# Performance work log

Measured on AMD Instinct MI355X. Metric: run time of the kernel, lower is better.

## Reference

```python
import jax, jax.numpy as jnp
import numpy as np

B, M, L, D, H, DFF, K, NL = 32, 512, 512, 128, 8, 256, 16, 2


def setup_inputs() -> dict:
    key = jax.random.key(0)
    ks = jax.random.split(key, 12)
    s = 0.02
    p = lambda i, shape: (jax.random.normal(ks[i], shape, jnp.float32) * s)
    return {
        "enc_out_vari": jax.random.normal(ks[0], (B, M, D), jnp.float32),
        "x_enc": jax.random.normal(ks[1], (B, L, M), jnp.float32),
        "conv1_W": p(2, (D, D)), "conv1_b": jnp.zeros((D,), jnp.float32),
        "conv2_W": p(3, (D, D)), "conv2_b": jnp.zeros((D,), jnp.float32),
        "Wq": p(4, (NL, D, D)), "Wk": p(5, (NL, D, D)),
        "Wv": p(6, (NL, D, D)), "Wo": p(7, (NL, D, D)),
        "ffn_W1": p(8, (NL, D, DFF)), "ffn_b1": jnp.zeros((NL, DFF), jnp.float32),
        "ffn_W2": p(9, (NL, DFF, D)), "ffn_b2": jnp.zeros((NL, D), jnp.float32),
        "ln1_g": jnp.ones((NL, D), jnp.float32), "ln1_b": jnp.zeros((NL, D), jnp.float32),
        "ln2_g": jnp.ones((NL, D), jnp.float32), "ln2_b": jnp.zeros((NL, D), jnp.float32),
    }


def _ln(x, g, b, eps=1e-5):
    mu = x.mean(-1, keepdims=True)
    var = ((x - mu) ** 2).mean(-1, keepdims=True)
    return (x - mu) * jax.lax.rsqrt(var + eps) * g + b


def _gcn_conv(x, src, dst, W, b, N):
    # PyG GCNConv: XW, add self loops, symmetric D^-1/2 (A+I) D^-1/2 aggregation, + bias
    h = x @ W
    loop = jnp.arange(N)
    s = jnp.concatenate([src, loop])
    d = jnp.concatenate([dst, loop])
    deg = jax.ops.segment_sum(jnp.ones_like(d, jnp.float32), d, num_segments=N)
    dinv = jnp.where(deg > 0, jax.lax.rsqrt(deg), 0.0)
    norm = dinv[s] * dinv[d]
    out = jax.ops.segment_sum(h[s] * norm[:, None], d, num_segments=N)
    return out + b


def _forward(enc_out_vari, x_enc, conv1_W, conv1_b, conv2_W, conv2_b,
             Wq, Wk, Wv, Wo, ffn_W1, ffn_b1, ffn_W2, ffn_b2,
             ln1_g, ln1_b, ln2_g, ln2_b):
    # --- dynamic graph from Pearson correlation (faithful: ascending argsort, idx 1..k) ---
    x = x_enc.transpose(0, 2, 1)                      # [B, M, L]
    c = x - x.mean(-1, keepdims=True)
    cov = jnp.einsum('bml,bnl->bmn', c, c) / (L - 1)  # [B, M, M]
    std = jnp.sqrt(jnp.diagonal(cov, axis1=-2, axis2=-1))
    std = jnp.where(std == 0, 1.0, std)
    corr = cov / (std[:, :, None] * std[:, None, :])
    neighbors = jnp.argsort(corr, axis=-1)[:, :, 1:K + 1]  # [B, M, K]
    row = jnp.tile(jnp.arange(M), K)                  # arange(M).repeat(k) in torch
    col = neighbors.reshape(B, M * K)
    offs = (jnp.arange(B) * M)[:, None]               # batch the graphs into one
    src = (row[None, :] + offs).reshape(-1)
    dst = (col + offs).reshape(-1)
    N = B * M
    # --- 2-layer GCN over flattened node set ---
    x_raw = enc_out_vari.reshape(N, D)
    h1 = jax.nn.relu(_gcn_conv(x_raw, src, dst, conv1_W, conv1_b, N))
    h2 = jax.nn.relu(_gcn_conv(h1, src, dst, conv2_W, conv2_b, N))
    xg = h2.reshape(B, M, D)
    # --- cross-attention transformer encoder: query stream = enc_out_vari, kv = GCN output ---
    h = enc_out_vari
    hd = D // H
    scale = 1.0 / jnp.sqrt(jnp.float32(hd))
    for l in range(NL):
        q = (h @ Wq[l]).reshape(B, M, H, hd)
        k_ = (xg @ Wk[l]).reshape(B, M, H, hd)
        v = (xg @ Wv[l]).reshape(B, M, H, hd)
        att = jax.nn.softmax(jnp.einsum('bqhd,bkhd->bhqk', q, k_) * scale, axis=-1)
        o = jnp.einsum('bhqk,bkhd->bqhd', att, v).reshape(B, M, D) @ Wo[l]
        h = _ln(h + o, ln1_g[l], ln1_b[l])
        f = jax.nn.relu(h @ ffn_W1[l] + ffn_b1[l]) @ ffn_W2[l] + ffn_b2[l]
        h = _ln(h + f, ln2_g[l], ln2_b[l])
    return h


def reference(enc_out_vari, x_enc, conv1_W, conv1_b, conv2_W, conv2_b,
              Wq, Wk, Wv, Wo, ffn_W1, ffn_b1, ffn_W2, ffn_b2,
              ln1_g, ln1_b, ln2_g, ln2_b):
    return _forward(enc_out_vari, x_enc, conv1_W, conv1_b, conv2_W, conv2_b,
                    Wq, Wk, Wv, Wo, ffn_W1, ffn_b1, ffn_W2, ffn_b2,
                    ln1_g, ln1_b, ln2_g, ln2_b)
```

## Files before the change

### kernel.cpp

```cpp
#include <hip/hip_runtime.h>
#include <float.h>

#define BB 32
#define MMv 512
#define LLv 512
#define DDv 128
#define HHv 8
#define DFFv 256
#define KNB 16
#define NLAY 2
#define NNODE (BB*MMv)
#define TOTE  (NNODE*KNB)
#define WTOT  294912

typedef unsigned short ushort_t;
typedef unsigned int u32;
typedef __attribute__((ext_vector_type(8))) short bf16x8;
typedef __attribute__((ext_vector_type(4))) float f32x4;

__device__ __forceinline__ float bf2f(ushort_t u){
  union { u32 i; float f; } x; x.i = ((u32)u) << 16; return x.f;
}
__device__ __forceinline__ ushort_t f2bf(float f){
  union { u32 i; float f; } x; x.f = f;
  u32 r = x.i + 0x7FFFu + ((x.i >> 16) & 1u);
  return (ushort_t)(r >> 16);
}
__device__ __forceinline__ float ldx(const void* p, size_t i, int f32){
  return f32 ? ((const float*)p)[i] : bf2f(((const ushort_t*)p)[i]);
}
__device__ __forceinline__ float wsum(float v){
  #pragma unroll
  for(int s=32;s;s>>=1) v += __shfl_xor(v,s);
  return v;
}

__global__ __launch_bounds__(256) void diag_fill_k(float* out, int n, float val){
  for(int i = blockIdx.x*256 + threadIdx.x; i < n; i += gridDim.x*256) out[i] = val;
}

struct P18 { const ushort_t* p[18]; int n[18]; };
__global__ __launch_bounds__(256) void ddet_k(P18 a, int* DF){
  int i = blockIdx.x;
  const ushort_t* q = a.p[i];
  int P = min(a.n[i], 4096);
  int t = threadIdx.x;
  int r1 = 0, evenNZ = 0, oddNZ = 0;
  for(int j=t; j<P; j+=256){
    ushort_t v = q[j];
    if(((v >> 7) & 0xFF) >= 0xC0) r1 = 1;
    if(v){ if(j & 1) oddNZ = 1; else evenNZ = 1; }
  }
  __shared__ int sh[3];
  if(t==0){ sh[0]=0; sh[1]=0; sh[2]=0; }
  __syncthreads();
  if(r1) atomicOr(&sh[0],1);
  if(evenNZ) atomicOr(&sh[1],1);
  if(oddNZ) atomicOr(&sh[2],1);
  __syncthreads();
  if(t==0) DF[i] = sh[0] | ((sh[1]==0) & (sh[2]!=0));
}

__global__ __launch_bounds__(256) void prep_k(const void* c1W, const void* c2W,
    const void* Wq, const void* Wk, const void* Wv, const void* Wo,
    const void* W1, const void* W2, ushort_t* Wth, ushort_t* Wtl, const int* DF){
  __shared__ ushort_t th[32][33];
  __shared__ ushort_t tl[32][33];
  int job = blockIdx.z;
  const void* src; int dfi; size_t soff, doff; int K, N;
  switch(job){
    case 0:  src=c1W; dfi=2;  soff=0; K=128; N=128; doff=0; break;
    case 1:  src=c2W; dfi=4;  soff=0; K=128; N=128; doff=16384; break;
    case 2: case 3:
      src=Wq; dfi=6; soff=(size_t)(job-2)*16384; K=128; N=128;
      doff=32768 + (size_t)(job-2)*16384; break;
    case 4: case 5:
      src=Wk; dfi=7; soff=(size_t)(job-4)*16384; K=128; N=128;
      doff=65536 + (size_t)(job-4)*16384; break;
    case 6: case 7:
      src=Wv; dfi=8; soff=(size_t)(job-6)*16384; K=128; N=128;
      doff=98304 + (size_t)(job-6)*16384; break;
    case 8: case 9:
      src=Wo; dfi=9; soff=(size_t)(job-8)*16384; K=128; N=128;
      doff=131072 + (size_t)(job-8)*16384; break;
    case 10: case 11:
      src=W1; dfi=10; soff=(size_t)(job-10)*32768; K=128; N=256;
      doff=163840 + (size_t)(job-10)*32768; break;
    default:
      src=W2; dfi=12; soff=(size_t)(job-12)*32768; K=256; N=128;
      doff=229376 + (size_t)(job-12)*32768; break;
  }
  int n0 = blockIdx.x*32, k0 = blockIdx.y*32;
  if(n0 >= N || k0 >= K) return;
  int f32 = DF[dfi];
  int tx = threadIdx.x, ty = threadIdx.y;
  #pragma unroll
  for(int i=0;i<4;i++){
    int k = k0+ty+8*i, n = n0+tx;
    float x = ldx(src, soff + (size_t)k*N + n, f32);
    ushort_t hi = f2bf(x);
    ushort_t lo = f2bf(x - bf2f(hi));
    th[ty+8*i][tx] = hi; tl[ty+8*i][tx] = lo;
  }
  __syncthreads();
  #pragma unroll
  for(int i=0;i<4;i++){
    int n = n0+ty+8*i, k = k0+tx;
    size_t d = doff + (size_t)n*K + k;
    Wth[d] = th[tx][ty+8*i];
    Wtl[d] = tl[tx][ty+8*i];
  }
}

__global__ __launch_bounds__(256) void split_k(const void* xe, ushort_t* Xhi,
                                               ushort_t* Xlo, const int* DF){
  __shared__ ushort_t th[32][33];
  __shared__ ushort_t tl[32][33];
  int f32 = DF[1];
  int b = blockIdx.z;
  int m0 = blockIdx.x*32, l0 = blockIdx.y*32;
  int tx = threadIdx.x, ty = threadIdx.y;
  #pragma unroll
  for(int i=0;i<4;i++){
    int l = l0+ty+8*i, m = m0+tx;
    float x = ldx(xe, (size_t)b*LLv*MMv + (size_t)l*MMv + m, f32);
    ushort_t hi = f2bf(x);
    ushort_t lo = f2bf(x - bf2f(hi));
    th[ty+8*i][tx] = hi; tl[ty+8*i][tx] = lo;
  }
  __syncthreads();
  #pragma unroll
  for(int i=0;i<4;i++){
    size_t d = (size_t)b*MMv*LLv + (size_t)(m0+ty+8*i)*LLv + l0+tx;
    Xhi[d] = th[tx][ty+8*i];
    Xlo[d] = tl[tx][ty+8*i];
  }
}

__global__ __launch_bounds__(256) void stats2_k(const ushort_t* Xhi, const ushort_t* Xlo,
                                                double* S64, double* R64){
  int row = blockIdx.x*4 + (threadIdx.x >> 6);
  int lane = threadIdx.x & 63;
  const ushort_t* Hr = Xhi + (size_t)row*LLv + lane*8;
  const ushort_t* Lr = Xlo + (size_t)row*LLv + lane*8;
  float s = 0.f, ss = 0.f;
  #pragma unroll
  for(int j=0;j<8;j++){
    float x = bf2f(Hr[j]) + bf2f(Lr[j]);
    s += x; ss = fmaf(x, x, ss);
  }
  s = wsum(s); ss = wsum(ss);
  if(lane == 0){
    S64[row] = (double)s;
    float cov = (ss - s*s*(1.0f/LLv)) * (1.0f/(LLv-1));
    float sd = (cov > 0.f) ? sqrtf(cov) : 0.f;
    R64[row] = (sd > 0.f) ? (double)(1.0f/sd) : 1.0;
  }
}

__global__ __launch_bounds__(1024) void corrsel_k(const ushort_t* Xhi, const ushort_t* Xlo,
                                                  const double* S64, const double* R64,
                                                  int* nbr, const int* DF){
  __shared__ __attribute__((aligned(16))) ushort_t Ah[32*520];
  __shared__ __attribute__((aligned(16))) ushort_t Al[32*520];
  __shared__ float Cs[32*516];
  int f32 = DF[1];
  int lin = blockIdx.y*16 + blockIdx.x;
  int xcd = lin & 7, slot = lin >> 3;
  int b = xcd + 8*(slot >> 4);
  int strip = slot & 15;
  int m0 = strip*32;
  int t = threadIdx.x;
  int wave = t >> 6, lane = t & 63;
  int quad = lane >> 4, l16 = lane & 15;
  const ushort_t* Hb = Xhi + (size_t)b*MMv*LLv;
  const ushort_t* Lb = Xlo + (size_t)b*MMv*LLv;
  for(int idx=t; idx<2048; idx+=1024){
    int mm = idx >> 6, c8 = (idx & 63)*8;
    *(bf16x8*)&Ah[mm*520 + c8] = *(const bf16x8*)&Hb[(size_t)(m0+mm)*LLv + c8];
    *(bf16x8*)&Al[mm*520 + c8] = *(const bf16x8*)&Lb[(size_t)(m0+mm)*LLv + c8];
  }
  __syncthreads();
  const double* Sb = S64 + b*MMv;
  const double* Rb = R64 + b*MMv;
  int nbase = wave*32;
  for(int cs=0; cs<2; cs++){
    int nn = nbase + cs*16 + l16;
    size_t brow = (size_t)nn*LLv + quad*8;
    f32x4 a00={0.f,0.f,0.f,0.f}, a01={0.f,0.f,0.f,0.f}, a02={0.f,0.f,0.f,0.f};
    f32x4 a10={0.f,0.f,0.f,0.f}, a11={0.f,0.f,0.f,0.f}, a12={0.f,0.f,0.f,0.f};
    if(f32){
      #pragma unroll
      for(int g=0; g<4; g++){
        bf16x8 bh[4], bl[4];
        #pragma unroll
        for(int j=0;j<4;j++) bh[j] = *(const bf16x8*)&Hb[brow + g*128 + j*32];
        #pragma unroll
        for(int j=0;j<4;j++) bl[j] = *(const bf16x8*)&Lb[brow + g*128 + j*32];
        #pragma unroll
        for(int j=0;j<4;j++){
          int ko = g*128 + j*32 + quad*8;
          bf16x8 ah0 = *(const bf16x8*)&Ah[l16*520 + ko];
          bf16x8 al0 = *(const bf16x8*)&Al[l16*520 + ko];
          bf16x8 ah1 = *(const bf16x8*)&Ah[(16+l16)*520 + ko];
          bf16x8 al1 = *(const bf16x8*)&Al[(16+l16)*520 + ko];
          a00 = __builtin_amdgcn_mfma_f32_16x16x32_bf16(ah0, bh[j], a00, 0, 0, 0);
          a01 = __builtin_amdgcn_mfma_f32_16x16x32_bf16(ah0, bl[j], a01, 0, 0, 0);
          a02 = __builtin_amdgcn_mfma_f32_16x16x32_bf16(al0, bh[j], a02, 0, 0, 0);
          a10 = __builtin_amdgcn_mfma_f32_16x16x32_bf16(ah1, bh[j], a10, 0, 0, 0);
          a11 = __builtin_amdgcn_mfma_f32_16x16x32_bf16(ah1, bl[j], a11, 0, 0, 0);
          a12 = __builtin_amdgcn_mfma_f32_16x16x32_bf16(al1, bh[j], a12, 0, 0, 0);
        }
      }
    } else {
      #pragma unroll
      for(int g=0; g<2; g++){
        bf16x8 bh[8];
        #pragma unroll
        for(int j=0;j<8;j++) bh[j] = *(const bf16x8*)&Hb[brow + g*256 + j*32];
        #pragma unroll
        for(int j=0;j<8;j++){
          int ko = g*256 + j*32 + quad*8;
          bf16x8 ah0 = *(const bf16x8*)&Ah[l16*520 + ko];
          bf16x8 ah1 = *(const bf16x8*)&Ah[(16+l16)*520 + ko];
          if(j & 1){
            a01 = __builtin_amdgcn_mfma_f32_16x16x32_bf16(ah0, bh[j], a01, 0, 0, 0);
            a11 = __builtin_amdgcn_mfma_f32_16x16x32_bf16(ah1, bh[j], a11, 0, 0, 0);
          } else {
            a00 = __builtin_amdgcn_mfma_f32_16x16x32_bf16(ah0, bh[j], a00, 0, 0, 0);
            a10 = __builtin_amdgcn_mfma_f32_16x16x32_bf16(ah1, bh[j], a10, 0, 0, 0);
          }
        }
      }
    }
    float sn = (float)(Sb[nn]*(1.0/LLv));
    float rn = (float)Rb[nn];
    #pragma unroll
    for(int r=0;r<4;r++){
      int ml0 = quad*4 + r;
      float s0 = a00[r] + a01[r] + a02[r];
      float cov0 = (s0 - (float)Sb[m0+ml0]*sn) * (1.0f/(LLv-1));
      Cs[ml0*516 + nn] = cov0 * (float)Rb[m0+ml0] * rn;
      int ml1 = 16 + ml0;
      float s1 = a10[r] + a11[r] + a12[r];
      float cov1 = (s1 - (float)Sb[m0+ml1]*sn) * (1.0f/(LLv-1));
      Cs[ml1*516 + nn] = cov1 * (float)Rb[m0+ml1] * rn;
    }
  }
  __syncthreads();
  for(int rr=0; rr<2; rr++){
    int r = wave*2 + rr;
    float vals[8];
    #pragma unroll
    for(int j=0;j<8;j++) vals[j] = Cs[r*516 + lane + 64*j];
    for(int it=0; it<=KNB; it++){
      float bvv = FLT_MAX; int bi = 0x7fffffff;
      #pragma unroll
      for(int j=0;j<8;j++){
        int n = lane + 64*j;
        if(vals[j] < bvv){ bvv = vals[j]; bi = n; }
      }
      #pragma unroll
      for(int s=32; s; s>>=1){
        float v2 = __shfl_xor(bvv, s);
        int   i2 = __shfl_xor(bi,  s);
        if(v2 < bvv || (v2 == bvv && i2 < bi)){ bvv = v2; bi = i2; }
      }
      int gbi = bi;
      int bic = min(max(gbi, 0), MMv-1);
      if(it > 0 && lane == 0) nbr[(size_t)(b*MMv + m0 + r)*KNB + it-1] = bic;
      if((gbi & 63) == lane && gbi < MMv){
        int jj = gbi >> 6;
        #pragma unroll
        for(int j=0;j<8;j++) if(j == jj) vals[j] = FLT_MAX;
      }
    }
  }
}

__global__ __launch_bounds__(256) void zero_k(int* p){
  p[blockIdx.x*256 + threadIdx.x] = 0;
}

__global__ __launch_bounds__(256) void hist_k(const int* nbr, int* cnt){
  int tid = blockIdx.x*256 + threadIdx.x;
  int b = tid >> 13;
  int col = min(max(nbr[tid], 0), MMv-1);
  atomicAdd(&cnt[b*MMv + col], 1);
}

__global__ __launch_bounds__(256) void scan_k(const int* cnt, int* off,
                                              int* cursor, float* dinv){
  __shared__ int part[256];
  int t = threadIdx.x;
  int base = t*64, s = 0;
  for(int i=0;i<64;i++) s += cnt[base+i];
  part[t] = s; __syncthreads();
  for(int st=1; st<256; st<<=1){
    int v = (t >= st) ? part[t-st] : 0;
    __syncthreads();
    part[t] += v; __syncthreads();
  }
  int run = (t > 0) ? part[t-1] : 0;
  for(int i=0;i<64;i++){
    int idx = base+i;
    off[idx] = run; cursor[idx] = run;
    run += cnt[idx];
    dinv[idx] = 1.0f/sqrtf((float)(cnt[idx]+1));
  }
  if(t == 255) off[NNODE] = run;
}

__global__ __launch_bounds__(256) void fill_k(const int* nbr, int* cursor, int* esrc){
  int tid = blockIdx.x*256 + threadIdx.x;
  int b = tid >> 13;
  int rem = tid & 8191;
  int col = min(max(nbr[tid], 0), MMv-1);
  int dst = b*MMv + col;
  int srcl = rem & 511;
  int pos = atomicAdd(&cursor[dst], 1);
  pos = min(max(pos, 0), TOTE-1);
  esrc[pos] = b*MMv + srcl;
}

__global__ __launch_bounds__(256) void gemm_k(const float* A,
                                              const ushort_t* Wth, const ushort_t* Wtl,
                                              size_t woffT, int wdi,
                                              const void* bias, int boff, int bdi,
                                              float* C, int Kd, int Dout, int relu,
                                              const int* DF){
  __shared__ __attribute__((aligned(16))) ushort_t Ah[64*72];
  __shared__ __attribute__((aligned(16))) ushort_t Al[64*72];
  __shared__ __attribute__((aligned(16))) ushort_t Wh[64*72];
  __shared__ __attribute__((aligned(16))) ushort_t Wl[64*72];
  int wf32 = DF[wdi];
  int bf32 = DF[bdi];
  int m0 = blockIdx.y*64, n0 = blockIdx.x*64;
  int t = threadIdx.x;
  int wave = t >> 6, lane = t & 63;
  int quad = lane >> 4, l16 = lane & 15;
  f32x4 acc[4];
  #pragma unroll
  for(int nt=0;nt<4;nt++) acc[nt] = (f32x4){0.f,0.f,0.f,0.f};
  for(int kc=0; kc<Kd; kc+=64){
    for(int s=t; s<1024; s+=256){
      int row = s >> 4, c4 = (s & 15)*4;
      float4 av = *(const float4*)&A[(size_t)(m0+row)*Kd + kc + c4];
      ushort_t h0=f2bf(av.x), h1=f2bf(av.y), h2=f2bf(av.z), h3=f2bf(av.w);
      ushort_t g0=f2bf(av.x-bf2f(h0)), g1=f2bf(av.y-bf2f(h1));
      ushort_t g2=f2bf(av.z-bf2f(h2)), g3=f2bf(av.w-bf2f(h3));
      *(ushort4*)&Ah[row*72 + c4] = make_ushort4(h0,h1,h2,h3);
      *(ushort4*)&Al[row*72 + c4] = make_ushort4(g0,g1,g2,g3);
    }
    for(int s=t; s<512; s+=256){
      int row = s >> 3, c8 = (s & 7)*8;
      size_t g = woffT + (size_t)(n0+row)*Kd + kc + c8;
      *(bf16x8*)&Wh[row*72 + c8] = *(const bf16x8*)&Wth[g];
      if(wf32) *(bf16x8*)&Wl[row*72 + c8] = *(const bf16x8*)&Wtl[g];
    }
    __syncthreads();
    #pragma unroll
    for(int kk=0; kk<64; kk+=32){
      int ko = kk + quad*8;
      bf16x8 ah = *(const bf16x8*)&Ah[(wave*16+l16)*72 + ko];
      bf16x8 al = *(const bf16x8*)&Al[(wave*16+l16)*72 + ko];
      #pragma unroll
      for(int nt=0; nt<4; nt++){
        bf16x8 wh = *(const bf16x8*)&Wh[(nt*16+l16)*72 + ko];
        acc[nt] = __builtin_amdgcn_mfma_f32_16x16x32_bf16(ah, wh, acc[nt], 0, 0, 0);
        acc[nt] = __builtin_amdgcn_mfma_f32_16x16x32_bf16(al, wh, acc[nt], 0, 0, 0);
        if(wf32){
          bf16x8 wl = *(const bf16x8*)&Wl[(nt*16+l16)*72 + ko];
          acc[nt] = __builtin_amdgcn_mfma_f32_16x16x32_bf16(ah, wl, acc[nt], 0, 0, 0);
        }
      }
    }
    __syncthreads();
  }
  #pragma unroll
  for(int nt=0; nt<4; nt++){
    int n = n0 + nt*16 + l16;
    float bv = bias ? ldx(bias, boff + n, bf32) : 0.f;
    #pragma unroll
    for(int r=0; r<4; r++){
      float v = acc[nt][r] + bv;
      if(relu) v = fmaxf(v, 0.f);
      C[(size_t)(m0 + wave*16 + quad*4 + r)*Dout + n] = v;
    }
  }
}

__global__ __launch_bounds__(256) void agg_k(const float* xw, const int* off,
                                             const int* esrc, const float* dinv,
                                             const void* bias, int bdi, float* out,
                                             const int* DF){
  int f32 = DF[bdi];
  int node = blockIdx.x*4 + (threadIdx.x >> 6);
  int lane = threadIdx.x & 63;
  float dn = dinv[node];
  float2 xv = ((const float2*)(xw + (size_t)node*DDv))[lane];
  float a0 = dn*dn*xv.x;
  float a1 = dn*dn*xv.y;
  int e0 = min(max(off[node], 0), TOTE);
  int e1 = min(max(off[node+1], e0), TOTE);
  for(int e=e0; e<e1; e++){
    int s = min(max(esrc[e], 0), NNODE-1);
    float w = dinv[s]*dn;
    float2 sv = ((const float2*)(xw + (size_t)s*DDv))[lane];
    a0 = fmaf(w, sv.x, a0);
    a1 = fmaf(w, sv.y, a1);
  }
  a0 += ldx(bias, 2*lane, f32); a1 += ldx(bias, 2*lane+1, f32);
  ((float2*)(out + (size_t)node*DDv))[lane] = make_float2(fmaxf(a0,0.f), fmaxf(a1,0.f));
}

__global__ __launch_bounds__(512) void attn_k(const float* qg, const float* kg,
                                              const float* vg, float* og){
  __shared__ float Ks[512*16];
  __shared__ float Vs[512*16];
  int bh = blockIdx.x;
  int b = bh >> 3, hh = bh & 7;
  size_t base = (size_t)b*MMv*DDv + (size_t)hh*16;
  int t = threadIdx.x;
  for(int idx=t; idx<2048; idx+=512){
    int kk = idx >> 2, i4 = (idx & 3)*4;
    ((float4*)Ks)[idx] = *(const float4*)&kg[base + (size_t)kk*DDv + i4];
    ((float4*)Vs)[idx] = *(const float4*)&vg[base + (size_t)kk*DDv + i4];
  }
  __syncthreads();
  int r = t;
  float qr[16];
  #pragma unroll
  for(int i4=0;i4<4;i4++){
    float4 qv = *(const float4*)&qg[base + (size_t)r*DDv + i4*4];
    qr[i4*4+0]=qv.x; qr[i4*4+1]=qv.y; qr[i4*4+2]=qv.z; qr[i4*4+3]=qv.w;
  }
  float m = -FLT_MAX, l = 0.f;
  float acc[16] = {};
  for(int kk=0; kk<512; kk++){
    const float* kp = &Ks[kk*16];
    float s = 0.f;
    #pragma unroll
    for(int i=0;i<16;i++) s = fmaf(qr[i], kp[i], s);
    s *= 0.25f;
    if(s > m){
      float c = __expf(m - s);
      l *= c;
      #pragma unroll
      for(int i=0;i<16;i++) acc[i] *= c;
      m = s;
    }
    float p = __expf(s - m);
    l += p;
    const float* vp = &Vs[kk*16];
    #pragma unroll
    for(int i=0;i<16;i++) acc[i] = fmaf(p, vp[i], acc[i]);
  }
  float inv = 1.0f/l;
  #pragma unroll
  for(int i=0;i<16;i++) og[base + (size_t)r*DDv + i] = acc[i]*inv;
}

__global__ __launch_bounds__(256) void ln_k(const float* h, const float* delta,
                                            const void* g, int gdi, const void* bb, int bdi, int po,
                                            float* dst, const int* DF){
  int gf32 = DF[gdi], bf32 = DF[bdi];
  int row = blockIdx.x*4 + (threadIdx.x >> 6);
  int lane = threadIdx.x & 63;
  const float2* hr = (const float2*)(h + (size_t)row*DDv);
  const float2* dr = (const float2*)(delta + (size_t)row*DDv);
  float2 hv = hr[lane], dv = dr[lane];
  float x0 = hv.x + dv.x, x1 = hv.y + dv.y;
  float mu = wsum(x0 + x1) * (1.0f/DDv);
  float d0 = x0 - mu, d1 = x1 - mu;
  float var = wsum(d0*d0 + d1*d1) * (1.0f/DDv);
  float rs = 1.0f/sqrtf(var + 1e-5f);
  int c0 = lane*2;
  float y0 = d0*rs*ldx(g, po+c0,   gf32) + ldx(bb, po+c0,   bf32);
  float y1 = d1*rs*ldx(g, po+c0+1, gf32) + ldx(bb, po+c0+1, bf32);
  ((float2*)(dst + (size_t)row*DDv))[lane] = make_float2(y0, y1);
}

__global__ __launch_bounds__(256) void cvt_k(const void* in, float* out, const int* DF){
  int f32 = DF[0];
  int tid = blockIdx.x*256 + threadIdx.x;
  out[tid] = ldx(in, tid, f32);
}

extern "C" void kernel_launch(void* const* d_in, const int* in_sizes, int n_in,
                              void* d_out, int out_size, void* d_ws, size_t ws_size,
                              hipStream_t stream) {
  if(n_in != 18){
    diag_fill_k<<<256, 256, 0, stream>>>((float*)d_out, out_size, 1000.0f);
    return;
  }
  const int expect[18] = {
    BB*MMv*DDv, BB*LLv*MMv, DDv*DDv, DDv, DDv*DDv, DDv,
    NLAY*DDv*DDv, NLAY*DDv*DDv, NLAY*DDv*DDv, NLAY*DDv*DDv,
    NLAY*DDv*DFFv, NLAY*DFFv, NLAY*DFFv*DDv, NLAY*DDv,
    NLAY*DDv, NLAY*DDv, NLAY*DDv, NLAY*DDv
  };
  for(int i=0;i<18;i++){
    if(in_sizes[i] != expect[i]){
      diag_fill_k<<<256, 256, 0, stream>>>((float*)d_out, out_size, 2000.0f + 10.0f*i);
      return;
    }
  }

  const void* enc  = d_in[0];
  const void* xe   = d_in[1];
  const void* c1W  = d_in[2];
  const void* c1b  = d_in[3];
  const void* c2W  = d_in[4];
  const void* c2b  = d_in[5];
  const void* Wq   = d_in[6];
  const void* Wk   = d_in[7];
  const void* Wv   = d_in[8];
  const void* Wo   = d_in[9];
  const void* W1   = d_in[10];
  const void* b1   = d_in[11];
  const void* W2   = d_in[12];
  const void* b2   = d_in[13];
  const void* ln1g = d_in[14];
  const void* ln1b = d_in[15];
  const void* ln2g = d_in[16];
  const void* ln2b = d_in[17];

  char* ws = (char*)d_ws;
  size_t o = 0;
  auto alloc = [&](size_t bytes){ size_t r = o; o = (o + bytes + 255) & ~(size_t)255; return r; };
  double* S64  = (double*)(ws + alloc((size_t)NNODE*8));
  double* R64  = (double*)(ws + alloc((size_t)NNODE*8));
  float* dinv  = (float*)(ws + alloc((size_t)NNODE*4));
  int*   cnt   = (int*)  (ws + alloc((size_t)NNODE*4));
  int*   cursor= (int*)  (ws + alloc((size_t)NNODE*4));
  int*   off   = (int*)  (ws + alloc((size_t)(NNODE+1)*4));
  int*   nbr   = (int*)  (ws + alloc((size_t)TOTE*4));
  int*   esrc  = (int*)  (ws + alloc((size_t)TOTE*4));
  int*   DF    = (int*)  (ws + alloc(256));
  ushort_t* Wth = (ushort_t*)(ws + alloc((size_t)WTOT*2));
  ushort_t* Wtl = (ushort_t*)(ws + alloc((size_t)WTOT*2));
  const size_t ACTF = (size_t)NNODE*DDv*4;
  float* hF = (float*)(ws + alloc(ACTF));
  float* xg = (float*)(ws + alloc(ACTF));
  float* t0 = (float*)(ws + alloc(ACTF));
  float* t1 = (float*)(ws + alloc(ACTF));
  float* t2 = (float*)(ws + alloc(ACTF));
  float* t3 = (float*)(ws + alloc(ACTF));
  float* fb = t1;
  ushort_t* Xhi = (ushort_t*)hF;
  ushort_t* Xlo = Xhi + (size_t)BB*MMv*LLv;
  if(ws_size < o){
    diag_fill_k<<<256, 256, 0, stream>>>((float*)d_out, out_size, 3000.0f);
    return;
  }

  P18 pack;
  for(int i=0;i<18;i++){ pack.p[i] = (const ushort_t*)d_in[i]; pack.n[i] = in_sizes[i]; }
  ddet_k<<<18, 256, 0, stream>>>(pack, DF);
  prep_k<<<dim3(8,8,14), dim3(32,8), 0, stream>>>(c1W, c2W, Wq, Wk, Wv, Wo, W1, W2,
                                                  Wth, Wtl, DF);

  split_k<<<dim3(16,16,BB), dim3(32,8), 0, stream>>>(xe, Xhi, Xlo, DF);
  stats2_k<<<NNODE/4, 256, 0, stream>>>(Xhi, Xlo, S64, R64);
  corrsel_k<<<dim3(16, BB), 1024, 0, stream>>>(Xhi, Xlo, S64, R64, nbr, DF);
  zero_k<<<NNODE/256, 256, 0, stream>>>(cnt);
  hist_k<<<TOTE/256, 256, 0, stream>>>(nbr, cnt);
  scan_k<<<1, 256, 0, stream>>>(cnt, off, cursor, dinv);
  fill_k<<<TOTE/256, 256, 0, stream>>>(nbr, cursor, esrc);

  cvt_k<<<NNODE*DDv/256, 256, 0, stream>>>(enc, hF, DF);
  gemm_k<<<dim3(2,256), 256, 0, stream>>>(hF, Wth, Wtl, 0, 2, nullptr, 0, 3, t0, DDv, DDv, 0, DF);
  agg_k<<<NNODE/4, 256, 0, stream>>>(t0, off, esrc, dinv, c1b, 3, t1, DF);
  gemm_k<<<dim3(2,256), 256, 0, stream>>>(t1, Wth, Wtl, 16384, 4, nullptr, 0, 5, t0, DDv, DDv, 0, DF);
  agg_k<<<NNODE/4, 256, 0, stream>>>(t0, off, esrc, dinv, c2b, 5, xg, DF);

  for(int l=0; l<NLAY; l++){
    gemm_k<<<dim3(2,256), 256, 0, stream>>>(hF, Wth, Wtl, 32768 + (size_t)l*16384, 6, nullptr, 0, 6, t0, DDv, DDv, 0, DF);
    gemm_k<<<dim3(2,256), 256, 0, stream>>>(xg, Wth, Wtl, 65536 + (size_t)l*16384, 7, nullptr, 0, 7, t1, DDv, DDv, 0, DF);
    gemm_k<<<dim3(2,256), 256, 0, stream>>>(xg, Wth, Wtl, 98304 + (size_t)l*16384, 8, nullptr, 0, 8, t2, DDv, DDv, 0, DF);
    attn_k<<<BB*HHv, 512, 0, stream>>>(t0, t1, t2, t3);
    gemm_k<<<dim3(2,256), 256, 0, stream>>>(t3, Wth, Wtl, 131072 + (size_t)l*16384, 9, nullptr, 0, 9, t0, DDv, DDv, 0, DF);
    ln_k<<<NNODE/4, 256, 0, stream>>>(hF, t0, ln1g, 14, ln1b, 15, l*DDv, hF, DF);
    gemm_k<<<dim3(4,256), 256, 0, stream>>>(hF, Wth, Wtl, 163840 + (size_t)l*32768, 10, b1, l*DFFv, 11, fb, DDv, DFFv, 1, DF);
    gemm_k<<<dim3(2,256), 256, 0, stream>>>(fb, Wth, Wtl, 229376 + (size_t)l*32768, 12, b2, l*DDv, 13, t0, DFFv, DDv, 0, DF);
    float* dst = (l == NLAY-1) ? (float*)d_out : hF;
    ln_k<<<NNODE/4, 256, 0, stream>>>(hF, t0, ln2g, 16, ln2b, 17, l*DDv, dst, DF);
  }
}
```

Measured before the change: 799.7 us.

## Fuse Q/K/V projections into one GEMM launch with interleaved KV layout

```diff
diff --git a/kernel.cpp b/kernel.cpp
--- a/kernel.cpp
+++ b/kernel.cpp
@@ -73,13 +73,13 @@
     case 1:  src=c2W; dfi=4;  soff=0; K=128; N=128; doff=16384; break;
     case 2: case 3:
       src=Wq; dfi=6; soff=(size_t)(job-2)*16384; K=128; N=128;
-      doff=32768 + (size_t)(job-2)*16384; break;
+      doff=32768 + (size_t)(job-2)*49152; break;
     case 4: case 5:
       src=Wk; dfi=7; soff=(size_t)(job-4)*16384; K=128; N=128;
-      doff=65536 + (size_t)(job-4)*16384; break;
+      doff=32768 + (size_t)(job-4)*49152 + 16384; break;
     case 6: case 7:
       src=Wv; dfi=8; soff=(size_t)(job-6)*16384; K=128; N=128;
-      doff=98304 + (size_t)(job-6)*16384; break;
+      doff=32768 + (size_t)(job-6)*49152 + 32768; break;
     case 8: case 9:
       src=Wo; dfi=9; soff=(size_t)(job-8)*16384; K=128; N=128;
       doff=131072 + (size_t)(job-8)*16384; break;
@@ -390,6 +390,72 @@
   }
 }
 
+__global__ __launch_bounds__(256) void qkv_k(const float* hF, const float* xg,
+                                             const ushort_t* Wth, const ushort_t* Wtl,
+                                             size_t qoff, float* t0, float* kv,
+                                             const int* DF){
+  __shared__ __attribute__((aligned(16))) ushort_t Ah[64*72];
+  __shared__ __attribute__((aligned(16))) ushort_t Al[64*72];
+  __shared__ __attribute__((aligned(16))) ushort_t Wh[64*72];
+  __shared__ __attribute__((aligned(16))) ushort_t Wl[64*72];
+  int m0 = blockIdx.y*64, n0 = blockIdx.x*64;
+  int wdi = (n0 < 128) ? 6 : ((n0 < 256) ? 7 : 8);
+  int wf32 = DF[wdi];
+  const float* A = (n0 < 128) ? hF : xg;
+  int t = threadIdx.x;
+  int wave = t >> 6, lane = t & 63;
+  int quad = lane >> 4, l16 = lane & 15;
+  f32x4 acc[4];
+  #pragma unroll
+  for(int nt=0;nt<4;nt++) acc[nt] = (f32x4){0.f,0.f,0.f,0.f};
+  for(int kc=0; kc<DDv; kc+=64){
+    for(int s=t; s<1024; s+=256){
+      int row = s >> 4, c4 = (s & 15)*4;
+      float4 av = *(const float4*)&A[(size_t)(m0+row)*DDv + kc + c4];
+      ushort_t h0=f2bf(av.x), h1=f2bf(av.y), h2=f2bf(av.z), h3=f2bf(av.w);
+      ushort_t g0=f2bf(av.x-bf2f(h0)), g1=f2bf(av.y-bf2f(h1));
+      ushort_t g2=f2bf(av.z-bf2f(h2)), g3=f2bf(av.w-bf2f(h3));
+      *(ushort4*)&Ah[row*72 + c4] = make_ushort4(h0,h1,h2,h3);
+      *(ushort4*)&Al[row*72 + c4] = make_ushort4(g0,g1,g2,g3);
+    }
+    for(int s=t; s<512; s+=256){
+      int row = s >> 3, c8 = (s & 7)*8;
+      size_t g = qoff + (size_t)(n0+row)*DDv + kc + c8;
+      *(bf16x8*)&Wh[row*72 + c8] = *(const bf16x8*)&Wth[g];
+      if(wf32) *(bf16x8*)&Wl[row*72 + c8] = *(const bf16x8*)&Wtl[g];
+    }
+    __syncthreads();
+    #pragma unroll
+    for(int kk=0; kk<64; kk+=32){
+      int ko = kk + quad*8;
+      bf16x8 ah = *(const bf16x8*)&Ah[(wave*16+l16)*72 + ko];
+      bf16x8 al = *(const bf16x8*)&Al[(wave*16+l16)*72 + ko];
+      #pragma unroll
+      for(int nt=0; nt<4; nt++){
+        bf16x8 wh = *(const bf16x8*)&Wh[(nt*16+l16)*72 + ko];
+        acc[nt] = __builtin_amdgcn_mfma_f32_16x16x32_bf16(ah, wh, acc[nt], 0, 0, 0);
+        acc[nt] = __builtin_amdgcn_mfma_f32_16x16x32_bf16(al, wh, acc[nt], 0, 0, 0);
+        if(wf32){
+          bf16x8 wl = *(const bf16x8*)&Wl[(nt*16+l16)*72 + ko];
+          acc[nt] = __builtin_amdgcn_mfma_f32_16x16x32_bf16(ah, wl, acc[nt], 0, 0, 0);
+        }
+      }
+    }
+    __syncthreads();
+  }
+  float* C = (n0 < 128) ? t0 : kv;
+  int ldC = (n0 < 128) ? 128 : 256;
+  int nb  = (n0 < 128) ? n0 : (n0 - 128);
+  #pragma unroll
+  for(int nt=0; nt<4; nt++){
+    int n = nb + nt*16 + l16;
+    #pragma unroll
+    for(int r=0; r<4; r++){
+      C[(size_t)(m0 + wave*16 + quad*4 + r)*ldC + n] = acc[nt][r];
+    }
+  }
+}
+
 __global__ __launch_bounds__(256) void agg_k(const float* xw, const int* off,
                                              const int* esrc, const float* dinv,
                                              const void* bias, int bdi, float* out,
@@ -403,7 +469,23 @@
   float a1 = dn*dn*xv.y;
   int e0 = min(max(off[node], 0), TOTE);
   int e1 = min(max(off[node+1], e0), TOTE);
-  for(int e=e0; e<e1; e++){
+  int e = e0;
+  for(; e + 4 <= e1; e += 4){
+    int s0 = min(max(esrc[e+0], 0), NNODE-1);
+    int s1 = min(max(esrc[e+1], 0), NNODE-1);
+    int s2 = min(max(esrc[e+2], 0), NNODE-1);
+    int s3 = min(max(esrc[e+3], 0), NNODE-1);
+    float2 v0 = ((const float2*)(xw + (size_t)s0*DDv))[lane];
+    float2 v1 = ((const float2*)(xw + (size_t)s1*DDv))[lane];
+    float2 v2 = ((const float2*)(xw + (size_t)s2*DDv))[lane];
+    float2 v3 = ((const float2*)(xw + (size_t)s3*DDv))[lane];
+    float w0 = dinv[s0]*dn, w1 = dinv[s1]*dn, w2 = dinv[s2]*dn, w3 = dinv[s3]*dn;
+    a0 = fmaf(w0, v0.x, a0); a1 = fmaf(w0, v0.y, a1);
+    a0 = fmaf(w1, v1.x, a0); a1 = fmaf(w1, v1.y, a1);
+    a0 = fmaf(w2, v2.x, a0); a1 = fmaf(w2, v2.y, a1);
+    a0 = fmaf(w3, v3.x, a0); a1 = fmaf(w3, v3.y, a1);
+  }
+  for(; e < e1; e++){
     int s = min(max(esrc[e], 0), NNODE-1);
     float w = dinv[s]*dn;
     float2 sv = ((const float2*)(xw + (size_t)s*DDv))[lane];
@@ -414,25 +496,26 @@
   ((float2*)(out + (size_t)node*DDv))[lane] = make_float2(fmaxf(a0,0.f), fmaxf(a1,0.f));
 }
 
-__global__ __launch_bounds__(512) void attn_k(const float* qg, const float* kg,
-                                              const float* vg, float* og){
+__global__ __launch_bounds__(512) void attn_k(const float* qg, const float* kv,
+                                              float* og){
   __shared__ float Ks[512*16];
   __shared__ float Vs[512*16];
   int bh = blockIdx.x;
   int b = bh >> 3, hh = bh & 7;
-  size_t base = (size_t)b*MMv*DDv + (size_t)hh*16;
+  size_t baseq = (size_t)b*MMv*DDv + (size_t)hh*16;
+  size_t basekv = (size_t)b*MMv*256 + (size_t)hh*16;
   int t = threadIdx.x;
   for(int idx=t; idx<2048; idx+=512){
     int kk = idx >> 2, i4 = (idx & 3)*4;
-    ((float4*)Ks)[idx] = *(const float4*)&kg[base + (size_t)kk*DDv + i4];
-    ((float4*)Vs)[idx] = *(const float4*)&vg[base + (size_t)kk*DDv + i4];
+    ((float4*)Ks)[idx] = *(const float4*)&kv[basekv + (size_t)kk*256 + i4];
+    ((float4*)Vs)[idx] = *(const float4*)&kv[basekv + (size_t)kk*256 + 128 + i4];
   }
   __syncthreads();
   int r = t;
   float qr[16];
   #pragma unroll
   for(int i4=0;i4<4;i4++){
-    float4 qv = *(const float4*)&qg[base + (size_t)r*DDv + i4*4];
+    float4 qv = *(const float4*)&qg[baseq + (size_t)r*DDv + i4*4];
     qr[i4*4+0]=qv.x; qr[i4*4+1]=qv.y; qr[i4*4+2]=qv.z; qr[i4*4+3]=qv.w;
   }
   float m = -FLT_MAX, l = 0.f;
@@ -458,7 +541,7 @@
   }
   float inv = 1.0f/l;
   #pragma unroll
-  for(int i=0;i<16;i++) og[base + (size_t)r*DDv + i] = acc[i]*inv;
+  for(int i=0;i<16;i++) og[baseq + (size_t)r*DDv + i] = acc[i]*inv;
 }
 
 __global__ __launch_bounds__(256) void ln_k(const float* h, const float* delta,
@@ -547,6 +630,7 @@
   float* t1 = (float*)(ws + alloc(ACTF));
   float* t2 = (float*)(ws + alloc(ACTF));
   float* t3 = (float*)(ws + alloc(ACTF));
+  float* kv = t1;
   float* fb = t1;
   ushort_t* Xhi = (ushort_t*)hF;
   ushort_t* Xlo = Xhi + (size_t)BB*MMv*LLv;
@@ -576,10 +660,9 @@
   agg_k<<<NNODE/4, 256, 0, stream>>>(t0, off, esrc, dinv, c2b, 5, xg, DF);
 
   for(int l=0; l<NLAY; l++){
-    gemm_k<<<dim3(2,256), 256, 0, stream>>>(hF, Wth, Wtl, 32768 + (size_t)l*16384, 6, nullptr, 0, 6, t0, DDv, DDv, 0, DF);
-    gemm_k<<<dim3(2,256), 256, 0, stream>>>(xg, Wth, Wtl, 65536 + (size_t)l*16384, 7, nullptr, 0, 7, t1, DDv, DDv, 0, DF);
-    gemm_k<<<dim3(2,256), 256, 0, stream>>>(xg, Wth, Wtl, 98304 + (size_t)l*16384, 8, nullptr, 0, 8, t2, DDv, DDv, 0, DF);
-    attn_k<<<BB*HHv, 512, 0, stream>>>(t0, t1, t2, t3);
+    qkv_k<<<dim3(6,256), 256, 0, stream>>>(hF, xg, Wth, Wtl,
+                                           32768 + (size_t)l*49152, t0, kv, DF);
+    attn_k<<<BB*HHv, 512, 0, stream>>>(t0, kv, t3);
     gemm_k<<<dim3(2,256), 256, 0, stream>>>(t3, Wth, Wtl, 131072 + (size_t)l*16384, 9, nullptr, 0, 9, t0, DDv, DDv, 0, DF);
     ln_k<<<NNODE/4, 256, 0, stream>>>(hF, t0, ln1g, 14, ln1b, 15, l*DDv, hF, DF);
     gemm_k<<<dim3(4,256), 256, 0, stream>>>(hF, Wth, Wtl, 163840 + (size_t)l*32768, 10, b1, l*DFFv, 11, fb, DDv, DFFv, 1, DF);
```

Result: faster. 748.1 us (-6.5%).
